# Kernel optimization log

Measured on AMD Instinct MI355X. Metric: run time of the kernel, lower is better.

Reference implementation:

```python
import jax, jax.numpy as jnp
import numpy as np

B, C, S, H, W, J = 4, 256, 256, 128, 128, 8
BN_EPS = 1e-5


def _conv3x3(x, w, b):
    # x: [B,S,H,W], w: [C,S,3,3] (OIHW), SAME padding, stride 1
    y = jax.lax.conv_general_dilated(x, w, window_strides=(1, 1), padding='SAME',
                                     dimension_numbers=('NCHW', 'OIHW', 'NCHW'))
    return y + b[None, :, None, None]


def setup_inputs() -> dict:
    key = jax.random.key(0)
    ks = jax.random.split(key, 12)
    fp = jax.random.normal(ks[0], (B, C, H, W), jnp.float32)
    labels = jax.random.randint(ks[1], (B, H, W), 0, J)
    sg = jax.nn.one_hot(labels, J, axis=1, dtype=jnp.float32)  # [B,J,H,W], disjoint masks
    style_codes = jax.random.normal(ks[2], (B, J + 1, S), jnp.float32)
    mask_codes = jax.random.randint(ks[3], (B, J), 0, 2)  # 0 or 1
    bn_gamma = 1.0 + 0.1 * jax.random.normal(ks[4], (C,), jnp.float32)
    bn_beta = 0.1 * jax.random.normal(ks[5], (C,), jnp.float32)
    W_mu = 0.05 * jax.random.normal(ks[6], (J, S, S), jnp.float32)
    b_mu = 0.05 * jax.random.normal(ks[7], (J, S), jnp.float32)
    W_gamma = 0.05 * jax.random.normal(ks[8], (C, S, 3, 3), jnp.float32)
    b_gamma = 0.05 * jax.random.normal(ks[9], (C,), jnp.float32)
    W_beta = 0.05 * jax.random.normal(ks[10], (C, S, 3, 3), jnp.float32)
    b_beta = 0.05 * jax.random.normal(ks[11], (C,), jnp.float32)
    return {"fp": fp, "sg": sg, "style_codes": style_codes, "mask_codes": mask_codes,
            "bn_gamma": bn_gamma, "bn_beta": bn_beta, "W_mu": W_mu, "b_mu": b_mu,
            "W_gamma": W_gamma, "b_gamma": b_gamma, "W_beta": W_beta, "b_beta": b_beta}


def reference(fp, sg, style_codes, mask_codes, bn_gamma, bn_beta,
              W_mu, b_mu, W_gamma, b_gamma, W_beta, b_beta):
    # BatchNorm2d (training mode, biased variance, affine)
    mean = jnp.mean(fp, axis=(0, 2, 3))
    var = jnp.mean(jnp.square(fp - mean[None, :, None, None]), axis=(0, 2, 3))
    nf = (fp - mean[None, :, None, None]) * jax.lax.rsqrt(var + BN_EPS)[None, :, None, None]
    nf = nf * bn_gamma[None, :, None, None] + bn_beta[None, :, None, None]

    # per-(batch,class) style code selection: j if mask_codes==1 else J (shared code)
    sel = jnp.where(mask_codes == 1, jnp.arange(J, dtype=mask_codes.dtype)[None, :], J)  # [B,J]
    codes = jnp.take_along_axis(style_codes, sel[:, :, None], axis=1)  # [B,J,S]

    # per-class FC + ReLU (torch Linear: y = x @ W.T + b)
    mu = jax.nn.relu(jnp.einsum('bjs,jos->bjo', codes, W_mu) + b_mu[None])  # [B,J,S]

    # scatter per-region style into spatial map (masks are disjoint one-hot)
    middle = jnp.einsum('bjhw,bjs->bshw', sg, mu)  # [B,S,H,W]

    gamma_avg = _conv3x3(middle, W_gamma, b_gamma)
    beta_avg = _conv3x3(middle, W_beta, b_beta)
    return nf * (1.0 + gamma_avg) + beta_avg
```

## Files before the change

kernel.cpp:

```cpp
#include <hip/hip_runtime.h>

#define Bb 4
#define Cc 256
#define Ss 256
#define Hh 128
#define Ww 128
#define Jj 8
#define HWp 16384
#define BN_EPS 1e-5f

#define WS_PS   0
#define WS_PQ   4096
#define WS_MU   10240
#define WS_LAB  43008
#define WS_WTG  108544
#define WS_WTB  2467840
#define WS_VT   4827136

#define VROW 144
#define SLICE_B 12288
#define SLICE_H 6144

typedef _Float16 h8 __attribute__((ext_vector_type(8)));

__global__ void k_prep(const float* __restrict__ fp, const float* __restrict__ sg,
                       const float* __restrict__ style, const int* __restrict__ mask,
                       const float* __restrict__ Wmu, const float* __restrict__ bmu,
                       const float* __restrict__ Wg, const float* __restrict__ Wb,
                       float* __restrict__ ws_f, unsigned char* __restrict__ labout,
                       float* __restrict__ muout,
                       float* __restrict__ wtg, float* __restrict__ wtb) {
    __shared__ float smem[1056];
    const int t = threadIdx.x;
    const int blk = blockIdx.x;
    if (blk < 1024) {
        const int c = blk >> 2, b = blk & 3;
        const float4* s4 = (const float4*)(fp + (size_t)(b * Cc + c) * HWp);
        float sum = 0.f, sq = 0.f;
        #pragma unroll
        for (int k = 0; k < 16; ++k) {
            float4 v = s4[t + k * 256];
            sum += v.x + v.y + v.z + v.w;
            sq  += v.x * v.x + v.y * v.y + v.z * v.z + v.w * v.w;
        }
        #pragma unroll
        for (int off = 32; off > 0; off >>= 1) {
            sum += __shfl_xor(sum, off);
            sq  += __shfl_xor(sq,  off);
        }
        const int lane = t & 63, wv = t >> 6;
        if (lane == 0) { smem[wv] = sum; smem[4 + wv] = sq; }
        __syncthreads();
        if (t == 0) {
            ws_f[blk]        = (smem[0] + smem[1]) + (smem[2] + smem[3]);
            ws_f[1024 + blk] = (smem[4] + smem[5]) + (smem[6] + smem[7]);
        }
    } else if (blk < 1280) {
        const int i = (blk - 1024) * 256 + t;
        const int b = i >> 14, p = i & (HWp - 1);
        const float* base = sg + (size_t)b * Jj * HWp + p;
        int l = 0;
        #pragma unroll
        for (int j = 0; j < Jj; ++j)
            if (base[(size_t)j * HWp] > 0.5f) l = j;
        labout[i] = (unsigned char)l;
    } else if (blk < 1312) {
        const int lb = blk - 1280;
        const int b = lb >> 3, j = lb & 7;
        const int sel = (mask[b * Jj + j] == 1) ? j : Jj;
        float* code = smem;
        code[t] = style[(size_t)(b * (Jj + 1) + sel) * Ss + t];
        __syncthreads();
        const float4* wrow = (const float4*)(Wmu + (size_t)(j * Ss + t) * Ss);
        const float4* c4 = (const float4*)code;
        float acc = bmu[j * Ss + t];
        #pragma unroll 8
        for (int s4i = 0; s4i < Ss / 4; ++s4i) {
            float4 w = wrow[s4i]; float4 cv = c4[s4i];
            acc += w.x * cv.x + w.y * cv.y + w.z * cv.z + w.w * cv.w;
        }
        muout[(size_t)lb * Ss + t] = fmaxf(acc, 0.f);
    } else {
        const int local = blk - 1312;
        const int z = local / 576;
        const int rem = local % 576;
        const int k0 = (rem % 72) * 32;
        const int r0 = (rem / 72) * 32;
        const float* in = z ? Wb : Wg;
        float* outp = z ? wtb : wtg;
        float (*tile)[33] = (float(*)[33])smem;
        const int tx = t & 31, ty = t >> 5;
        #pragma unroll
        for (int i2 = 0; i2 < 4; ++i2)
            tile[ty + 8 * i2][tx] = in[(size_t)(r0 + ty + 8 * i2) * 2304 + k0 + tx];
        __syncthreads();
        #pragma unroll
        for (int i2 = 0; i2 < 4; ++i2)
            outp[(size_t)(k0 + ty + 8 * i2) * 256 + r0 + tx] = tile[tx][ty + 8 * i2];
    }
}

__global__ void k_build(const float* __restrict__ bn_g, const float* __restrict__ bn_b,
                        const float* __restrict__ bgam, const float* __restrict__ bbet,
                        const float* __restrict__ wtg, const float* __restrict__ wtb,
                        const float* __restrict__ mu, float* __restrict__ ws_f,
                        _Float16* __restrict__ vt) {
    const int t = threadIdx.x;
    if (blockIdx.x == 0) {
        if (t < 256) {
            float s = 0.f, q = 0.f;
            #pragma unroll
            for (int b = 0; b < 4; ++b) { s += ws_f[t * 4 + b]; q += ws_f[1024 + t * 4 + b]; }
            float mean = s * (1.f / 65536.f);
            float var  = q * (1.f / 65536.f) - mean * mean;
            float sc = bn_g[t] * rsqrtf(var + BN_EPS);
            float sh = bn_b[t] - mean * sc;
            ((float4*)ws_f)[t] = make_float4(sc, sh, 1.f + bgam[t], bbet[t]);
        }
        return;
    }
    const int lb = blockIdx.x - 1;
    const int z = lb / 36;
    const int rem = lb % 36;
    const int tap = rem % 9, b = rem / 9;
    const float* Wt = z ? wtb : wtg;
    const int c = t & 255;
    const int sq = __builtin_amdgcn_readfirstlane(t >> 8);
    const float* mub = mu + (size_t)b * Jj * Ss;
    float ag[8] = {0,0,0,0,0,0,0,0};
    const float* wp = Wt + (size_t)tap * 256 + c;
    #pragma unroll 16
    for (int si = 0; si < 64; ++si) {
        const int s = sq * 64 + si;
        const float wv = wp[(size_t)s * 2304];
        #pragma unroll
        for (int j = 0; j < 8; ++j) ag[j] += wv * mub[j * 256 + s];
    }
    __shared__ float red[4][256][9];
    #pragma unroll
    for (int j = 0; j < 8; ++j) red[sq][c][j] = ag[j];
    __syncthreads();
    if (sq != 0) return;
    #pragma unroll
    for (int j = 0; j < 8; ++j)
        ag[j] = (red[0][c][j] + red[1][c][j]) + (red[2][c][j] + red[3][c][j]);
    const int cc = c >> 5, cl = c & 31;
    _Float16* base = vt + (size_t)(cc * 4 + b) * SLICE_H + z * 32 + cl;
    #pragma unroll
    for (int j = 0; j < 8; ++j) base[(tap * 9 + j) * 72] = (_Float16)ag[j];
    base[(tap * 9 + 8) * 72] = (_Float16)0.f;
}

__global__ void __launch_bounds__(256, 4) k_main(
    const float* __restrict__ fp, const unsigned char* __restrict__ lab,
    const char* __restrict__ vt, const float4* __restrict__ T,
    float* __restrict__ out) {
    const int h0 = blockIdx.x * 2, cc = blockIdx.y, b = blockIdx.z;
    __shared__ __align__(16) char vbuf[SLICE_B];
    __shared__ int labs[4][132];
    const int t = threadIdx.x;
    const int lane = t & 63;
    const int wid = __builtin_amdgcn_readfirstlane(t >> 6);

    {
        const char* slice = vt + (size_t)(cc * 4 + b) * SLICE_B;
        for (int r = wid; r < 12; r += 4) {
            __builtin_amdgcn_global_load_lds(
                (const __attribute__((address_space(1))) void*)(slice + r * 1024 + lane * 16),
                (__attribute__((address_space(3))) void*)(vbuf + r * 1024), 16, 0, 0);
        }
    }
    for (int idx = t; idx < 4 * 132; idx += 256) {
        const int r = idx / 132, col = idx % 132 - 1;
        const int hh = h0 - 1 + r;
        int v = 8;
        if (hh >= 0 && hh < Hh && col >= 0 && col < Ww)
            v = lab[((size_t)b << 14) + (hh << 7) + col];
        labs[r][idx % 132] = v;
    }
    __syncthreads();

    const int w = t & 127;
    const int cs = __builtin_amdgcn_readfirstlane(t >> 7);
    const int cbase = cc * 32 + cs * 16;
    const float4* Tw = T + cbase;

    for (int hh = 0; hh < 2; ++hh) {
        int vb0[9];
        #pragma unroll
        for (int tap = 0; tap < 9; ++tap) {
            const int j = labs[hh + tap / 3][w + tap % 3];
            vb0[tap] = (tap * 9 + j) * VROW + cs * 32;
        }
        const size_t io = ((size_t)(b * Cc + cbase) << 14) + ((h0 + hh) << 7) + w;
        const float* fpp = fp + io;
        float* outp = out + io;
        float f[16];
        #pragma unroll
        for (int lc = 0; lc < 16; ++lc)
            f[lc] = __builtin_nontemporal_load(fpp + (size_t)lc * HWp);
        __builtin_amdgcn_sched_barrier(0);
        #pragma unroll
        for (int cb = 0; cb < 2; ++cb) {
            h8 vg[9];
            #pragma unroll
            for (int tap = 0; tap < 9; ++tap)
                vg[tap] = *(const h8*)(vbuf + vb0[tap] + cb * 16);
            __builtin_amdgcn_sched_barrier(0);
            h8 ve[9];
            #pragma unroll
            for (int tap = 0; tap < 9; ++tap)
                ve[tap] = *(const h8*)(vbuf + vb0[tap] + 64 + cb * 16);
            h8 gab = (vg[0] + vg[1]) + (vg[2] + vg[3]);
            h8 gcd = (vg[4] + vg[5]) + (vg[6] + vg[7]);
            h8 g8 = vg[8];
            __builtin_amdgcn_sched_barrier(0);
            h8 eab = (ve[0] + ve[1]) + (ve[2] + ve[3]);
            h8 ecd = (ve[4] + ve[5]) + (ve[6] + ve[7]);
            h8 e8 = ve[8];
            #pragma unroll
            for (int i = 0; i < 8; ++i) {
                const int lc = cb * 8 + i;
                const float4 tv = Tw[lc];
                const float g = ((float)gab[i] + (float)gcd[i]) + (float)g8[i];
                const float e = ((float)eab[i] + (float)ecd[i]) + (float)e8[i];
                const float nf = fmaf(f[lc], tv.x, tv.y);
                const float res = fmaf(nf, tv.z + g, tv.w + e);
                __builtin_nontemporal_store(res, outp + (size_t)lc * HWp);
            }
        }
    }
}

extern "C" void kernel_launch(void* const* d_in, const int* in_sizes, int n_in,
                              void* d_out, int out_size, void* d_ws, size_t ws_size,
                              hipStream_t stream) {
    const float* fp      = (const float*)d_in[0];
    const float* sg      = (const float*)d_in[1];
    const float* style   = (const float*)d_in[2];
    const int*   mask    = (const int*)d_in[3];
    const float* bn_g    = (const float*)d_in[4];
    const float* bn_b    = (const float*)d_in[5];
    const float* W_mu    = (const float*)d_in[6];
    const float* b_mu    = (const float*)d_in[7];
    const float* W_gam   = (const float*)d_in[8];
    const float* b_gam   = (const float*)d_in[9];
    const float* W_bet   = (const float*)d_in[10];
    const float* b_bet   = (const float*)d_in[11];
    float* out = (float*)d_out;

    char* ws = (char*)d_ws;
    float*         ws_f  = (float*)ws;
    unsigned char* labp  = (unsigned char*)(ws + WS_LAB);
    float*         mup   = (float*)(ws + WS_MU);
    float*         wtg   = (float*)(ws + WS_WTG);
    float*         wtb   = (float*)(ws + WS_WTB);
    _Float16*      vtp   = (_Float16*)(ws + WS_VT);

    k_prep<<<2464, 256, 0, stream>>>(fp, sg, style, mask, W_mu, b_mu, W_gam, W_bet,
                                     ws_f, labp, mup, wtg, wtb);
    k_build<<<73, 1024, 0, stream>>>(bn_g, bn_b, b_gam, b_bet, wtg, wtb, mup, ws_f, vtp);
    k_main<<<dim3(64, 8, 4), 256, 0, stream>>>(fp, labp, (const char*)vtp,
                                               (const float4*)ws_f, out);
}
```

Baseline: 59.61 us.

## Process four rows per block and software-pipeline fp loads across channel halves

Each k_main block now handles four output rows instead of two, halving the grid and reusing the per-block LDS slice load across more rows. The fp loads are split into two 8-channel halves that are double-buffered: the next half is issued before the current half's compute, and the first load is issued before the barrier. The goal is to hide global load latency and amortize setup. In exchange there is less parallelism (1024 blocks) and a larger label tile.

Result: slower. 92.71 us (+55.5%).

```diff
diff --git a/kernel.cpp b/kernel.cpp
--- a/kernel.cpp
+++ b/kernel.cpp
@@ -155,9 +155,9 @@
     const float* __restrict__ fp, const unsigned char* __restrict__ lab,
     const char* __restrict__ vt, const float4* __restrict__ T,
     float* __restrict__ out) {
-    const int h0 = blockIdx.x * 2, cc = blockIdx.y, b = blockIdx.z;
+    const int h0 = blockIdx.x * 4, cc = blockIdx.y, b = blockIdx.z;
     __shared__ __align__(16) char vbuf[SLICE_B];
-    __shared__ int labs[4][132];
+    __shared__ int labs[6][132];
     const int t = threadIdx.x;
     const int lane = t & 63;
     const int wid = __builtin_amdgcn_readfirstlane(t >> 6);
@@ -170,7 +170,7 @@
                 (__attribute__((address_space(3))) void*)(vbuf + r * 1024), 16, 0, 0);
         }
     }
-    for (int idx = t; idx < 4 * 132; idx += 256) {
+    for (int idx = t; idx < 6 * 132; idx += 256) {
         const int r = idx / 132, col = idx % 132 - 1;
         const int hh = h0 - 1 + r;
         int v = 8;
@@ -178,55 +178,92 @@
             v = lab[((size_t)b << 14) + (hh << 7) + col];
         labs[r][idx % 132] = v;
     }
-    __syncthreads();
 
     const int w = t & 127;
     const int cs = __builtin_amdgcn_readfirstlane(t >> 7);
     const int cbase = cc * 32 + cs * 16;
     const float4* Tw = T + cbase;
-
-    for (int hh = 0; hh < 2; ++hh) {
+    const size_t io0 = ((size_t)(b * Cc + cbase) << 14) + (h0 << 7) + w;
+    const float* fpp = fp + io0;
+    float* outp = out + io0;
+
+    float fA[8], fB[8];
+    #pragma unroll
+    for (int i = 0; i < 8; ++i)
+        fA[i] = __builtin_nontemporal_load(fpp + (size_t)i * HWp);
+    __syncthreads();
+
+    #pragma unroll
+    for (int hh = 0; hh < 4; ++hh) {
         int vb0[9];
         #pragma unroll
         for (int tap = 0; tap < 9; ++tap) {
             const int j = labs[hh + tap / 3][w + tap % 3];
             vb0[tap] = (tap * 9 + j) * VROW + cs * 32;
         }
-        const size_t io = ((size_t)(b * Cc + cbase) << 14) + ((h0 + hh) << 7) + w;
-        const float* fpp = fp + io;
-        float* outp = out + io;
-        float f[16];
-        #pragma unroll
-        for (int lc = 0; lc < 16; ++lc)
-            f[lc] = __builtin_nontemporal_load(fpp + (size_t)lc * HWp);
-        __builtin_amdgcn_sched_barrier(0);
-        #pragma unroll
-        for (int cb = 0; cb < 2; ++cb) {
+        const float* fprow = fpp + (hh << 7);
+        float* outrow = outp + (hh << 7);
+
+        {
             h8 vg[9];
             #pragma unroll
             for (int tap = 0; tap < 9; ++tap)
-                vg[tap] = *(const h8*)(vbuf + vb0[tap] + cb * 16);
+                vg[tap] = *(const h8*)(vbuf + vb0[tap]);
             __builtin_amdgcn_sched_barrier(0);
             h8 ve[9];
             #pragma unroll
             for (int tap = 0; tap < 9; ++tap)
-                ve[tap] = *(const h8*)(vbuf + vb0[tap] + 64 + cb * 16);
+                ve[tap] = *(const h8*)(vbuf + vb0[tap] + 64);
+            #pragma unroll
+            for (int i = 0; i < 8; ++i)
+                fB[i] = __builtin_nontemporal_load(fprow + (size_t)(8 + i) * HWp);
+            __builtin_amdgcn_sched_barrier(0);
             h8 gab = (vg[0] + vg[1]) + (vg[2] + vg[3]);
             h8 gcd = (vg[4] + vg[5]) + (vg[6] + vg[7]);
             h8 g8 = vg[8];
-            __builtin_amdgcn_sched_barrier(0);
             h8 eab = (ve[0] + ve[1]) + (ve[2] + ve[3]);
             h8 ecd = (ve[4] + ve[5]) + (ve[6] + ve[7]);
             h8 e8 = ve[8];
             #pragma unroll
             for (int i = 0; i < 8; ++i) {
-                const int lc = cb * 8 + i;
-                const float4 tv = Tw[lc];
+                const float4 tv = Tw[i];
                 const float g = ((float)gab[i] + (float)gcd[i]) + (float)g8[i];
                 const float e = ((float)eab[i] + (float)ecd[i]) + (float)e8[i];
-                const float nf = fmaf(f[lc], tv.x, tv.y);
-                const float res = fmaf(nf, tv.z + g, tv.w + e);
-                __builtin_nontemporal_store(res, outp + (size_t)lc * HWp);
+                const float nf = fmaf(fA[i], tv.x, tv.y);
+                __builtin_nontemporal_store(fmaf(nf, tv.z + g, tv.w + e),
+                                            outrow + (size_t)i * HWp);
+            }
+        }
+        {
+            h8 vg[9];
+            #pragma unroll
+            for (int tap = 0; tap < 9; ++tap)
+                vg[tap] = *(const h8*)(vbuf + vb0[tap] + 16);
+            __builtin_amdgcn_sched_barrier(0);
+            h8 ve[9];
+            #pragma unroll
+            for (int tap = 0; tap < 9; ++tap)
+                ve[tap] = *(const h8*)(vbuf + vb0[tap] + 80);
+            if (hh < 3) {
+                #pragma unroll
+                for (int i = 0; i < 8; ++i)
+                    fA[i] = __builtin_nontemporal_load(fprow + 128 + (size_t)i * HWp);
+            }
+            __builtin_amdgcn_sched_barrier(0);
+            h8 gab = (vg[0] + vg[1]) + (vg[2] + vg[3]);
+            h8 gcd = (vg[4] + vg[5]) + (vg[6] + vg[7]);
+            h8 g8 = vg[8];
+            h8 eab = (ve[0] + ve[1]) + (ve[2] + ve[3]);
+            h8 ecd = (ve[4] + ve[5]) + (ve[6] + ve[7]);
+            h8 e8 = ve[8];
+            #pragma unroll
+            for (int i = 0; i < 8; ++i) {
+                const float4 tv = Tw[8 + i];
+                const float g = ((float)gab[i] + (float)gcd[i]) + (float)g8[i];
+                const float e = ((float)eab[i] + (float)ecd[i]) + (float)e8[i];
+                const float nf = fmaf(fB[i], tv.x, tv.y);
+                __builtin_nontemporal_store(fmaf(nf, tv.z + g, tv.w + e),
+                                            outrow + (size_t)(8 + i) * HWp);
             }
         }
     }
@@ -260,6 +297,6 @@
     k_prep<<<2464, 256, 0, stream>>>(fp, sg, style, mask, W_mu, b_mu, W_gam, W_bet,
                                      ws_f, labp, mup, wtg, wtb);
     k_build<<<73, 1024, 0, stream>>>(bn_g, bn_b, b_gam, b_bet, wtg, wtb, mup, ws_f, vtp);
-    k_main<<<dim3(64, 8, 4), 256, 0, stream>>>(fp, labp, (const char*)vtp,
+    k_main<<<dim3(32, 8, 4), 256, 0, stream>>>(fp, labp, (const char*)vtp,
                                                (const float4*)ws_f, out);
 }
```
